# Performance work log

Hardware: AMD Instinct MI355X
Metric: run time of the kernel (lower is better)

## Reference

```python
import jax, jax.numpy as jnp
import numpy as np

P = 2_000_000   # total gathered points (N1+N2+... after pillar grouping)
C_IN = 10       # mlps[0]: point feats + pillar-center offsets
C_OUT = 64      # mlps[1]
M = 200_000     # number of non-empty pillars (pillar_indices.shape[0])
BN_EPS = 1e-3


def setup_inputs() -> dict:
    key = jax.random.key(0)
    k0, k1, k2, k3, k4 = jax.random.split(key, 5)
    return {
        "group_features": jax.random.normal(k0, (P, C_IN), dtype=jnp.float32),
        "pillar_set_indices": jax.random.randint(k1, (P,), 0, M, dtype=jnp.int32),
        "num_pillars": M,
        # Linear(bias=False) weight, xavier-ish scale; stored (C_IN, C_OUT) so fwd is x @ W
        "W": jax.random.normal(k2, (C_IN, C_OUT), dtype=jnp.float32) * np.float32(1.0 / np.sqrt(C_IN)),
        "gamma": jnp.ones((C_OUT,), dtype=jnp.float32),
        "beta": jnp.zeros((C_OUT,), dtype=jnp.float32),
        "running_mean": jax.random.normal(k3, (C_OUT,), dtype=jnp.float32) * 0.1,
        "running_var": jax.random.uniform(k4, (C_OUT,), dtype=jnp.float32, minval=0.5, maxval=1.5),
    }


def reference(group_features, pillar_set_indices, num_pillars, W, gamma, beta, running_mean, running_var):
    # shared MLP: Linear(bias=False) -> BatchNorm1d(eval, eps=1e-3) -> ReLU
    h = group_features @ W                                   # (P, C_OUT)
    inv_std = gamma * jax.lax.rsqrt(running_var + BN_EPS)    # fold BN scale
    h = jax.nn.relu(h * inv_std + (beta - running_mean * inv_std))
    # scatter_max segment pooling into pillars; empty pillars -> 0 (ReLU output >= 0)
    pooled = jax.ops.segment_max(h, pillar_set_indices, num_segments=num_pillars)
    pillar_features = jnp.maximum(pooled, jnp.float32(0.0))  # (M, C_OUT)
    return pillar_features
```

## Files before the change

kernel.cpp:

```cpp
#include <hip/hip_runtime.h>


#define C_IN   10
#define C_OUT  64
#define BSHIFT 7
#define BPILL  128
#define MAXNBP 2048
#define NREG   8
#define SBLK   256
#define SCHUNK 4096
#define PPT    (SCHUNK / SBLK)
#define PBLK   512
#define SENT   (128u << 24)

typedef _Float16 half8 __attribute__((ext_vector_type(8)));
typedef float    f32x4 __attribute__((ext_vector_type(4)));

__device__ __attribute__((noinline))
void fallback_point(int p, int m, const float* gf, const float* W,
                    const float* gamma, const float* beta,
                    const float* rmean, const float* rvar,
                    float* out, int* ovf) {
    atomicExch(ovf, 1);
    const float* x = gf + (size_t)p * C_IN;
    unsigned* o = (unsigned*)out + (size_t)m * C_OUT;
#pragma clang loop unroll(disable)
    for (int c = 0; c < C_OUT; ++c) {
        float is = gamma[c] * rsqrtf(rvar[c] + 1e-3f);
        float bb = fmaf(-rmean[c], is, beta[c]);
        float d = 0.f;
        for (int k = 0; k < C_IN; ++k) d = fmaf(x[k], W[k * C_OUT + c], d);
        atomicMax(o + c, __float_as_uint(fmaxf(fmaf(d, is, bb), 0.f)));
    }
}

__global__ __launch_bounds__(SBLK)
void k_scatter(const int* __restrict__ idx,
               const float* __restrict__ gf,
               const float* __restrict__ W,
               const float* __restrict__ gamma,
               const float* __restrict__ beta,
               const float* __restrict__ rmean,
               const float* __restrict__ rvar,
               int* __restrict__ cnt, int* __restrict__ ovf,
               unsigned int* __restrict__ sorted,
               float* __restrict__ out,
               int P, int NBpad, int CAPR) {
    __shared__ int lh[MAXNBP];
    __shared__ int rbase[MAXNBP];
    const int t = threadIdx.x;
    const int r = blockIdx.x & (NREG - 1);

    for (int b = t; b < NBpad; b += SBLK) lh[b] = 0;
    __syncthreads();

    const int base = blockIdx.x * SCHUNK;
    int mm[PPT], rk[PPT];
#pragma unroll
    for (int i = 0; i < PPT; ++i) {
        int p = base + i * SBLK + t;
        mm[i] = (p < P) ? idx[p] : -1;
        rk[i] = (mm[i] >= 0) ? atomicAdd(&lh[mm[i] >> BSHIFT], 1) : 0;
    }
    __syncthreads();

    int* crow = cnt + (size_t)r * NBpad;
    for (int b = t; b < NBpad; b += SBLK) {
        int h = lh[b];
        rbase[b] = h ? atomicAdd(&crow[b], h) : 0;
    }
    __syncthreads();

#pragma unroll
    for (int i = 0; i < PPT; ++i) {
        if (mm[i] < 0) continue;
        int p = base + i * SBLK + t;
        int b = mm[i] >> BSHIFT;
        int slot = rbase[b] + rk[i];
        if (slot < CAPR) {
            sorted[((size_t)b * NREG + r) * CAPR + slot] =
                (unsigned)p | ((unsigned)(mm[i] & (BPILL - 1)) << 24);
        } else {
            fallback_point(p, mm[i], gf, W, gamma, beta, rmean, rvar, out, ovf);
        }
    }
}

__global__ __launch_bounds__(PBLK, 8)
void k_pool(const float* __restrict__ gf,
            const unsigned int* __restrict__ sorted,
            const int* __restrict__ cnt,
            const int* __restrict__ ovf,
            const float* __restrict__ W,
            const float* __restrict__ gamma,
            const float* __restrict__ beta,
            const float* __restrict__ rmean,
            const float* __restrict__ rvar,
            float* __restrict__ out, int M, int NBpad, int CAPR) {
    __shared__ unsigned int acc[129 * 65];
    const int t = threadIdx.x;
    const int lane = t & 63;
    const int wv = t >> 6;
    const int n = lane & 15;
    const int q = lane >> 4;

    for (int i = t; i < 129 * 65; i += PBLK) acc[i] = 0u;

    half8 bfrag[4];
    float inv[4], bia[4];
#pragma unroll
    for (int tt = 0; tt < 4; ++tt) {
        int c = tt * 16 + n;
#pragma unroll
        for (int j = 0; j < 8; ++j) {
            int k = q * 8 + j;
            bfrag[tt][j] = (k < C_IN) ? (_Float16)W[k * C_OUT + c] : (_Float16)0.f;
        }
        float is = gamma[c] * rsqrtf(rvar[c] + 1e-3f);
        inv[tt] = is;
        bia[tt] = fmaf(-rmean[c], is, beta[c]);
    }
    __syncthreads();

    const int blk = blockIdx.x;
    const int cn = min(cnt[(size_t)wv * NBpad + blk], CAPR);
    const unsigned int* src0 = sorted + ((size_t)blk * NREG + wv) * CAPR;
    const float2* gf2 = (const float2*)gf;

    for (int rb = 0; rb < cn; rb += 64) {
        unsigned v = (rb + lane < cn) ? src0[rb + lane] : SENT;
        const float2* src = gf2 + (size_t)(v & 0xFFFFFFu) * 5;
        float2 x0 = src[0], x1 = src[1], x2 = src[2], x3 = src[3], x4 = src[4];
        int u0 = __builtin_bit_cast(int, __builtin_amdgcn_cvt_pkrtz(x0.x, x0.y));
        int u1 = __builtin_bit_cast(int, __builtin_amdgcn_cvt_pkrtz(x1.x, x1.y));
        int u2 = __builtin_bit_cast(int, __builtin_amdgcn_cvt_pkrtz(x2.x, x2.y));
        int u3 = __builtin_bit_cast(int, __builtin_amdgcn_cvt_pkrtz(x3.x, x3.y));
        int u4 = __builtin_bit_cast(int, __builtin_amdgcn_cvt_pkrtz(x4.x, x4.y));

        const int ng = min(4, ((cn - rb) + 15) >> 4);
#pragma unroll
        for (int g = 0; g < 4; ++g) {
            if (g >= ng) break;
            const int sl = (g << 4) + n;
            int b0 = __shfl(u0, sl, 64);
            int b1 = __shfl(u1, sl, 64);
            int b2 = __shfl(u2, sl, 64);
            int b3 = __shfl(u3, sl, 64);
            int b4 = __shfl(u4, sl, 64);
            int4 a32;
            a32.x = (q == 0) ? b0 : ((q == 1) ? b4 : 0);
            a32.y = (q == 0) ? b1 : 0;
            a32.z = (q == 0) ? b2 : 0;
            a32.w = (q == 0) ? b3 : 0;
            half8 a = __builtin_bit_cast(half8, a32);
            f32x4 z = {0.f, 0.f, 0.f, 0.f};
            f32x4 d0 = __builtin_amdgcn_mfma_f32_16x16x32_f16(a, bfrag[0], z, 0, 0, 0);
            f32x4 d1 = __builtin_amdgcn_mfma_f32_16x16x32_f16(a, bfrag[1], z, 0, 0, 0);
            f32x4 d2 = __builtin_amdgcn_mfma_f32_16x16x32_f16(a, bfrag[2], z, 0, 0, 0);
            f32x4 d3 = __builtin_amdgcn_mfma_f32_16x16x32_f16(a, bfrag[3], z, 0, 0, 0);
#pragma unroll
            for (int r = 0; r < 4; ++r) {
                int pv = __shfl((int)v, (g << 4) + (q << 2) + r, 64);
                int abase = (int)(((unsigned)pv) >> 24) * 65 + n;
                float h0 = fmaxf(fmaf(d0[r], inv[0], bia[0]), 0.f);
                float h1 = fmaxf(fmaf(d1[r], inv[1], bia[1]), 0.f);
                float h2 = fmaxf(fmaf(d2[r], inv[2], bia[2]), 0.f);
                float h3 = fmaxf(fmaf(d3[r], inv[3], bia[3]), 0.f);
                atomicMax(&acc[abase +  0], __float_as_uint(h0));
                atomicMax(&acc[abase + 16], __float_as_uint(h1));
                atomicMax(&acc[abase + 32], __float_as_uint(h2));
                atomicMax(&acc[abase + 48], __float_as_uint(h3));
            }
        }
    }
    __syncthreads();

    const int anyovf = ovf[0];
    const int mbase = blk * BPILL;
#pragma unroll
    for (int i = 0; i < (BPILL * C_OUT) / PBLK; ++i) {
        int wdx = i * PBLK + t;
        int row = wdx >> 6, c = wdx & 63;
        int m = mbase + row;
        if (m < M) {
            unsigned uv = acc[row * 65 + c];
            if (anyovf) atomicMax((unsigned*)out + (size_t)m * C_OUT + c, uv);
            else        out[(size_t)m * C_OUT + c] = __uint_as_float(uv);
        }
    }
}

extern "C" void kernel_launch(void* const* d_in, const int* in_sizes, int n_in,
                              void* d_out, int out_size, void* d_ws, size_t ws_size,
                              hipStream_t stream) {
    const float* gf    = (const float*)d_in[0];
    const int*   idx   = (const int*)  d_in[1];
    const float* W     = (const float*)d_in[3];
    const float* gamma = (const float*)d_in[4];
    const float* beta  = (const float*)d_in[5];
    const float* rmean = (const float*)d_in[6];
    const float* rvar  = (const float*)d_in[7];
    float*       out   = (float*)d_out;

    const int P  = in_sizes[0] / C_IN;
    const int M  = out_size / C_OUT;
    const int NB    = (M + BPILL - 1) >> BSHIFT;
    const int NBpad = (NB + 32) & ~31;
    const int E     = NREG * NBpad;
    const int NSB   = (P + SCHUNK - 1) / SCHUNK;

    char* ws = (char*)d_ws;
    auto align256 = [](size_t x) { return (x + 255) & ~(size_t)255; };
    int* cnt = (int*)ws;  ws += align256((size_t)E * 4);
    int* ovf = (int*)ws;  ws += 256;
    unsigned int* sorted = (unsigned int*)ws;

    int CAPR = 512;
    size_t fixed = (size_t)((char*)sorted - (char*)cnt);
    while (CAPR > 128 && fixed + (size_t)E * CAPR * 4 > ws_size) CAPR -= 128;

    hipMemsetAsync(cnt, 0, fixed, stream);

    k_scatter<<<NSB, SBLK, 0, stream>>>(idx, gf, W, gamma, beta, rmean, rvar,
                                        cnt, ovf, sorted, out, P, NBpad, CAPR);
    k_pool   <<<NB,  PBLK, 0, stream>>>(gf, sorted, cnt, ovf, W, gamma, beta,
                                        rmean, rvar, out, M, NBpad, CAPR);
}
```

Before: 215.8 us.

## Carry packed fp16 point payloads through scatter instead of point indices

When the workspace is large enough, the scatter kernel reads each point's features coalesced, packs them to fp16, and writes a 24-byte payload (features plus local pillar id) into the bucketed array in SoA layout. The pool kernel then reads these payloads contiguously instead of doing a random gather from the feature array through a 4-byte index. This removes the random gather in the pool stage but adds payload write and read traffic and lowers per-bucket capacity to 240, which raises the chance of hitting the atomic fallback path. The old index path remains as a fallback when the workspace is small.

Measured after the change: 295.9 us. +37.1%, slower.

```diff
diff --git a/kernel.cpp b/kernel.cpp
--- a/kernel.cpp
+++ b/kernel.cpp
@@ -11,10 +11,12 @@
 #define SCHUNK 4096
 #define PPT    (SCHUNK / SBLK)
 #define PBLK   512
+#define TRASH  128
 #define SENT   (128u << 24)
 
 typedef _Float16 half8 __attribute__((ext_vector_type(8)));
 typedef float    f32x4 __attribute__((ext_vector_type(4)));
+typedef unsigned long long u64;
 
 __device__ __attribute__((noinline))
 void fallback_point(int p, int m, const float* gf, const float* W,
@@ -34,6 +36,7 @@
     }
 }
 
+template <bool PAY>
 __global__ __launch_bounds__(SBLK)
 void k_scatter(const int* __restrict__ idx,
                const float* __restrict__ gf,
@@ -43,9 +46,9 @@
                const float* __restrict__ rmean,
                const float* __restrict__ rvar,
                int* __restrict__ cnt, int* __restrict__ ovf,
-               unsigned int* __restrict__ sorted,
+               u64* __restrict__ pay, unsigned* __restrict__ tok,
                float* __restrict__ out,
-               int P, int NBpad, int CAPR) {
+               int P, int NBpad, int CAPR, size_t PS) {
     __shared__ int lh[MAXNBP];
     __shared__ int rbase[MAXNBP];
     const int t = threadIdx.x;
@@ -71,6 +74,7 @@
     }
     __syncthreads();
 
+    const float2* gf2 = (const float2*)gf;
 #pragma unroll
     for (int i = 0; i < PPT; ++i) {
         if (mm[i] < 0) continue;
@@ -78,17 +82,34 @@
         int b = mm[i] >> BSHIFT;
         int slot = rbase[b] + rk[i];
         if (slot < CAPR) {
-            sorted[((size_t)b * NREG + r) * CAPR + slot] =
-                (unsigned)p | ((unsigned)(mm[i] & (BPILL - 1)) << 24);
+            size_t off = ((size_t)b * NREG + r) * CAPR + slot;
+            if constexpr (PAY) {
+                const float2* src = gf2 + (size_t)p * 5;
+                float2 x0 = src[0], x1 = src[1], x2 = src[2];
+                float2 x3 = src[3], x4 = src[4];
+                unsigned u0 = __builtin_bit_cast(unsigned, __builtin_amdgcn_cvt_pkrtz(x0.x, x0.y));
+                unsigned u1 = __builtin_bit_cast(unsigned, __builtin_amdgcn_cvt_pkrtz(x1.x, x1.y));
+                unsigned u2 = __builtin_bit_cast(unsigned, __builtin_amdgcn_cvt_pkrtz(x2.x, x2.y));
+                unsigned u3 = __builtin_bit_cast(unsigned, __builtin_amdgcn_cvt_pkrtz(x3.x, x3.y));
+                unsigned u4 = __builtin_bit_cast(unsigned, __builtin_amdgcn_cvt_pkrtz(x4.x, x4.y));
+                pay[off]          = (u64)u0 | ((u64)u1 << 32);
+                pay[off + PS]     = (u64)u2 | ((u64)u3 << 32);
+                pay[off + 2 * PS] = (u64)u4 |
+                    ((u64)(unsigned)(mm[i] & (BPILL - 1)) << 32);
+            } else {
+                tok[off] = (unsigned)p | ((unsigned)(mm[i] & (BPILL - 1)) << 24);
+            }
         } else {
             fallback_point(p, mm[i], gf, W, gamma, beta, rmean, rvar, out, ovf);
         }
     }
 }
 
+template <bool PAY>
 __global__ __launch_bounds__(PBLK, 8)
 void k_pool(const float* __restrict__ gf,
-            const unsigned int* __restrict__ sorted,
+            const u64* __restrict__ pay,
+            const unsigned* __restrict__ tok,
             const int* __restrict__ cnt,
             const int* __restrict__ ovf,
             const float* __restrict__ W,
@@ -96,7 +117,7 @@
             const float* __restrict__ beta,
             const float* __restrict__ rmean,
             const float* __restrict__ rvar,
-            float* __restrict__ out, int M, int NBpad, int CAPR) {
+            float* __restrict__ out, int M, int NBpad, int CAPR, size_t PS) {
     __shared__ unsigned int acc[129 * 65];
     const int t = threadIdx.x;
     const int lane = t & 63;
@@ -124,18 +145,34 @@
 
     const int blk = blockIdx.x;
     const int cn = min(cnt[(size_t)wv * NBpad + blk], CAPR);
-    const unsigned int* src0 = sorted + ((size_t)blk * NREG + wv) * CAPR;
+    const size_t cbase = ((size_t)blk * NREG + wv) * CAPR;
     const float2* gf2 = (const float2*)gf;
 
     for (int rb = 0; rb < cn; rb += 64) {
-        unsigned v = (rb + lane < cn) ? src0[rb + lane] : SENT;
-        const float2* src = gf2 + (size_t)(v & 0xFFFFFFu) * 5;
-        float2 x0 = src[0], x1 = src[1], x2 = src[2], x3 = src[3], x4 = src[4];
-        int u0 = __builtin_bit_cast(int, __builtin_amdgcn_cvt_pkrtz(x0.x, x0.y));
-        int u1 = __builtin_bit_cast(int, __builtin_amdgcn_cvt_pkrtz(x1.x, x1.y));
-        int u2 = __builtin_bit_cast(int, __builtin_amdgcn_cvt_pkrtz(x2.x, x2.y));
-        int u3 = __builtin_bit_cast(int, __builtin_amdgcn_cvt_pkrtz(x3.x, x3.y));
-        int u4 = __builtin_bit_cast(int, __builtin_amdgcn_cvt_pkrtz(x4.x, x4.y));
+        int slot = rb + lane;
+        int u0, u1, u2, u3, u4, ml;
+        if constexpr (PAY) {
+            u64 w0 = 0, w1 = 0, w2 = ((u64)TRASH) << 32;
+            if (slot < cn) {
+                w0 = pay[cbase + slot];
+                w1 = pay[cbase + slot + PS];
+                w2 = pay[cbase + slot + 2 * PS];
+            }
+            u0 = (int)(unsigned)w0; u1 = (int)(unsigned)(w0 >> 32);
+            u2 = (int)(unsigned)w1; u3 = (int)(unsigned)(w1 >> 32);
+            u4 = (int)(unsigned)w2; ml = (int)(unsigned)(w2 >> 32);
+        } else {
+            unsigned v = (slot < cn) ? tok[cbase + slot] : SENT;
+            const float2* src = gf2 + (size_t)(v & 0xFFFFFFu) * 5;
+            float2 x0 = src[0], x1 = src[1], x2 = src[2];
+            float2 x3 = src[3], x4 = src[4];
+            u0 = __builtin_bit_cast(int, __builtin_amdgcn_cvt_pkrtz(x0.x, x0.y));
+            u1 = __builtin_bit_cast(int, __builtin_amdgcn_cvt_pkrtz(x1.x, x1.y));
+            u2 = __builtin_bit_cast(int, __builtin_amdgcn_cvt_pkrtz(x2.x, x2.y));
+            u3 = __builtin_bit_cast(int, __builtin_amdgcn_cvt_pkrtz(x3.x, x3.y));
+            u4 = __builtin_bit_cast(int, __builtin_amdgcn_cvt_pkrtz(x4.x, x4.y));
+            ml = (int)(v >> 24);
+        }
 
         const int ng = min(4, ((cn - rb) + 15) >> 4);
 #pragma unroll
@@ -160,8 +197,8 @@
             f32x4 d3 = __builtin_amdgcn_mfma_f32_16x16x32_f16(a, bfrag[3], z, 0, 0, 0);
 #pragma unroll
             for (int r = 0; r < 4; ++r) {
-                int pv = __shfl((int)v, (g << 4) + (q << 2) + r, 64);
-                int abase = (int)(((unsigned)pv) >> 24) * 65 + n;
+                int mlr = __shfl(ml, (g << 4) + (q << 2) + r, 64);
+                int abase = mlr * 65 + n;
                 float h0 = fmaxf(fmaf(d0[r], inv[0], bia[0]), 0.f);
                 float h1 = fmaxf(fmaf(d1[r], inv[1], bia[1]), 0.f);
                 float h2 = fmaxf(fmaf(d2[r], inv[2], bia[2]), 0.f);
@@ -213,16 +250,33 @@
     auto align256 = [](size_t x) { return (x + 255) & ~(size_t)255; };
     int* cnt = (int*)ws;  ws += align256((size_t)E * 4);
     int* ovf = (int*)ws;  ws += 256;
-    unsigned int* sorted = (unsigned int*)ws;
-
-    int CAPR = 512;
-    size_t fixed = (size_t)((char*)sorted - (char*)cnt);
-    while (CAPR > 128 && fixed + (size_t)E * CAPR * 4 > ws_size) CAPR -= 128;
+    char* arr = ws;
+    size_t fixed = (size_t)(arr - (char*)cnt);
+    size_t avail = (ws_size > fixed) ? ws_size - fixed : 0;
+
+    int CAPR;
+    bool paym;
+    if ((size_t)E * 240 * 24 <= avail) {
+        paym = true;  CAPR = 240;
+    } else {
+        paym = false; CAPR = 512;
+        while (CAPR > 128 && (size_t)E * CAPR * 4 > avail) CAPR -= 128;
+    }
+    const size_t PS = (size_t)E * CAPR;
+    u64*      pay = (u64*)arr;
+    unsigned* tok = (unsigned*)arr;
 
     hipMemsetAsync(cnt, 0, fixed, stream);
 
-    k_scatter<<<NSB, SBLK, 0, stream>>>(idx, gf, W, gamma, beta, rmean, rvar,
-                                        cnt, ovf, sorted, out, P, NBpad, CAPR);
-    k_pool   <<<NB,  PBLK, 0, stream>>>(gf, sorted, cnt, ovf, W, gamma, beta,
-                                        rmean, rvar, out, M, NBpad, CAPR);
-}
+    if (paym) {
+        k_scatter<true ><<<NSB, SBLK, 0, stream>>>(idx, gf, W, gamma, beta,
+            rmean, rvar, cnt, ovf, pay, tok, out, P, NBpad, CAPR, PS);
+        k_pool  <true ><<<NB,  PBLK, 0, stream>>>(gf, pay, tok, cnt, ovf, W,
+            gamma, beta, rmean, rvar, out, M, NBpad, CAPR, PS);
+    } else {
+        k_scatter<false><<<NSB, SBLK, 0, stream>>>(idx, gf, W, gamma, beta,
+            rmean, rvar, cnt, ovf, pay, tok, out, P, NBpad, CAPR, PS);
+        k_pool  <false><<<NB,  PBLK, 0, stream>>>(gf, pay, tok, cnt, ovf, W,
+            gamma, beta, rmean, rvar, out, M, NBpad, CAPR, PS);
+    }
+}
```
